# Performance work log

Hardware: AMD Instinct MI355X
Metric: run time of the kernel (lower is better)

Reference implementation:

```python
import jax, jax.numpy as jnp
import numpy as np

POOLED_H = 7
POOLED_W = 7
SPATIAL_SCALE = 0.0625
B, C, H, W = 8, 256, 48, 48
R = 300
IMG = 768  # = H / SPATIAL_SCALE


def setup_inputs() -> dict:
    key = jax.random.key(0)
    k1, k2, k3, k4 = jax.random.split(key, 4)
    features = jax.random.normal(k1, (B, C, H, W), dtype=jnp.float32)
    # rois: (batch_idx, x1, y1, x2, y2) in input-image coords
    bidx = jax.random.randint(k2, (R, 1), 0, B).astype(jnp.float32)
    tl = jax.random.uniform(k3, (R, 2), minval=0.0, maxval=IMG - 64.0)
    wh = jax.random.uniform(k4, (R, 2), minval=32.0, maxval=320.0)
    br = jnp.minimum(tl + wh, IMG - 1.0)
    rois = jnp.concatenate([bidx, tl, br], axis=1).astype(jnp.float32)
    return {"features": features, "rois": rois}


def _hat_integral(x, grid):
    """Integral from -inf to x of the unit hat basis function centered at each
    grid point g (support [g-1, g+1], peak 1, total mass 1).
    x: [..., 1-broadcastable], grid: [G] -> returns [..., G]."""
    t = x[..., None] - (grid - 1.0)
    return jnp.where(
        t <= 0.0, 0.0,
        jnp.where(t <= 1.0, 0.5 * t * t,
                  jnp.where(t <= 2.0, 1.0 - 0.5 * (2.0 - t) ** 2, 1.0)))


def reference(features, rois):
    # Precise RoI Pooling: exact double integral of the bilinear interpolant
    # over each bin, divided by bin area. Bilinear interp (with zero padding
    # outside the map, as in the CUDA PrRoIPoolingGetData) is
    #   f(u,v) = sum_{j,i} feat[j,i] * hat_j(v) * hat_i(u)
    # so the bin integral factorizes into per-axis hat-integral weights.
    Bf, Cf, Hf, Wf = features.shape
    bidx = rois[:, 0].astype(jnp.int32)
    x1 = rois[:, 1] * SPATIAL_SCALE
    y1 = rois[:, 2] * SPATIAL_SCALE
    x2 = rois[:, 3] * SPATIAL_SCALE
    y2 = rois[:, 4] * SPATIAL_SCALE
    roi_w = jnp.maximum(x2 - x1, 0.0)
    roi_h = jnp.maximum(y2 - y1, 0.0)
    bin_w = roi_w / POOLED_W  # [R]
    bin_h = roi_h / POOLED_H

    ph = jnp.arange(POOLED_H, dtype=jnp.float32)
    pw = jnp.arange(POOLED_W, dtype=jnp.float32)
    ya = y1[:, None] + ph[None, :] * bin_h[:, None]  # [R, PH]
    yb = ya + bin_h[:, None]
    xa = x1[:, None] + pw[None, :] * bin_w[:, None]  # [R, PW]
    xb = xa + bin_w[:, None]

    gy = jnp.arange(Hf, dtype=jnp.float32)
    gx = jnp.arange(Wf, dtype=jnp.float32)
    Wy = _hat_integral(yb, gy) - _hat_integral(ya, gy)  # [R, PH, H]
    Wx = _hat_integral(xb, gx) - _hat_integral(xa, gx)  # [R, PW, W]

    feat = features[bidx]  # [R, C, H, W]
    t = jnp.einsum('rpj,rcji->rcpi', Wy, feat)   # integrate over y
    num = jnp.einsum('rqi,rcpi->rcpq', Wx, t)    # integrate over x -> [R,C,PH,PW]

    area = (bin_w * bin_h)[:, None, None, None]  # win_size per ROI
    out = jnp.where(area > 0.0, num / jnp.where(area > 0.0, area, 1.0), 0.0)
    return out
```

## Files before the change

kernel.cpp:

```cpp
#include <hip/hip_runtime.h>


#define PH 7
#define PW 7
#define NBINS 49
#define SCALE 0.0625f
#define CH 256
#define FH 48
#define FW 48
#define RNUM 300
#define CB 8
#define QN 2
#define MAXJ 23
#define ROWF 28
#define PRM 112

__device__ __forceinline__ float hat_int(float x, float g) {
    float t = x - (g - 1.0f);
    if (t <= 0.0f) return 0.0f;
    if (t <= 1.0f) return 0.5f * t * t;
    if (t <= 2.0f) { float u = 2.0f - t; return 1.0f - 0.5f * u * u; }
    return 1.0f;
}

__global__ __launch_bounds__(256)
void prroi_prep(const float* __restrict__ rois, float* __restrict__ prm) {
    const int r = blockIdx.x * 4 + (threadIdx.x >> 6);
    const int t = threadIdx.x & 63;
    if (r >= RNUM || t >= 15) return;

    const float* roi = rois + r * 5;
    const int   b  = (int)roi[0];
    const float x1 = roi[1] * SCALE, y1 = roi[2] * SCALE;
    const float x2 = roi[3] * SCALE, y2 = roi[4] * SCALE;
    const float roi_w = fmaxf(x2 - x1, 0.0f), roi_h = fmaxf(y2 - y1, 0.0f);
    const float bin_w = roi_w / (float)PW, bin_h = roi_h / (float)PH;
    const float area = bin_w * bin_h;
    const float inv_area = (area > 0.0f) ? (1.0f / area) : 0.0f;

    const float ylo = fminf(y1, y2), yhi = fmaxf(y1, y2);
    const float xlo = fminf(x1, x2), xhi = fmaxf(x1, x2);
    const int j1 = min(FH - 1, (int)floorf(yhi) + 1);
    const int i1 = min(FW - 1, (int)floorf(xhi) + 1);
    const int J0 = min(max(0, (int)floorf(ylo) - 1), FH - 6);
    const int I0 = min(max(0, (int)floorf(xlo) - 1) & ~3, FW - 8);
    const int JROWS = min(FH - J0, max(j1 - J0 + 1, 6));
    int NI4 = min(((i1 - I0) >> 2) + 1, (FW - I0) >> 2);
    NI4 = max(NI4, 2);

    float* p = prm + (size_t)r * PRM;
    if (t < PH) {
        const int ph = t;
        const float ya = y1 + ph * bin_h, yb = ya + bin_h;
        const int base = min(max((int)floorf(ya) - 1, J0), J0 + JROWS - 6);
        p[84 + ph] = __int_as_float(base - J0);
#pragma unroll
        for (int k = 0; k < 6; ++k) {
            const float g = (float)(base + k);
            p[ph * 6 + k] = hat_int(yb, g) - hat_int(ya, g);
        }
    } else if (t < PH + PW) {
        const int pw = t - PH;
        const float xa = x1 + pw * bin_w, xb = xa + bin_w;
        const int base = min(max((int)floorf(xa) - 1, I0), I0 + 4 * NI4 - 6);
        p[91 + pw] = __int_as_float(base - I0);
#pragma unroll
        for (int k = 0; k < 6; ++k) {
            const float g = (float)(base + k);
            p[42 + pw * 6 + k] = hat_int(xb, g) - hat_int(xa, g);
        }
    } else {
        p[98]  = inv_area;
        p[99]  = __int_as_float(b);
        p[100] = __int_as_float(J0);
        p[101] = __int_as_float(I0);
        p[102] = __int_as_float(JROWS);
        p[103] = __int_as_float(NI4);
    }
}

__global__ __launch_bounds__(256)
void prroi_main(const float* __restrict__ feat,
                const float* __restrict__ prm,
                float* __restrict__ out) {
    const int cblk = blockIdx.x;
    const int r    = blockIdx.y;
    const int c0   = cblk * CB;
    const int tid  = threadIdx.x;

    __shared__ float patch[MAXJ * ROWF * CB];
    __shared__ float rs[PW * MAXJ * CB];

    const float* p = prm + (size_t)r * PRM;
    const int b     = __float_as_int(p[99]);
    const int J0    = __float_as_int(p[100]);
    const int I0    = __float_as_int(p[101]);
    const int JROWS = __float_as_int(p[102]);
    const int NI4   = __float_as_int(p[103]);

    const int nA = JROWS * 14;
    const int v1 = tid, v2 = tid + 256;
    int pw1 = 0, q1 = 0, j1r = 0, pw2 = 0, q2 = 0, j2r = 0, bi1 = 0, bi2 = 0;
    float wxa[6], wxb[6];
    const bool a1 = v1 < nA, a2 = v2 < nA;
    if (a1) {
        j1r = v1 / 14; const int rem = v1 - j1r * 14; pw1 = rem >> 1; q1 = rem & 1;
        bi1 = __float_as_int(p[91 + pw1]);
#pragma unroll
        for (int k = 0; k < 6; ++k) wxa[k] = p[42 + pw1 * 6 + k];
    }
    if (a2) {
        j2r = v2 / 14; const int rem = v2 - j2r * 14; pw2 = rem >> 1; q2 = rem & 1;
        bi2 = __float_as_int(p[91 + pw2]);
#pragma unroll
        for (int k = 0; k < 6; ++k) wxb[k] = p[42 + pw2 * 6 + k];
    }

    const int bin = tid & 63;
    const int cp  = tid >> 6;
    float wy[6]; int bj = 0, phv = 0, pwv = 0;
    float inv_area = p[98];
    if (bin < NBINS) {
        phv = bin / PW; pwv = bin - phv * PW;
        bj = __float_as_int(p[84 + phv]);
#pragma unroll
        for (int k = 0; k < 6; ++k) wy[k] = p[phv * 6 + k];
    }

    const float* fb = feat + (size_t)(b * CH + c0) * FH * FW;
    for (int u = tid; u < QN * MAXJ * 7; u += 256) {
        const int q   = u / (MAXJ * 7);
        const int rem = u - q * (MAXJ * 7);
        const int j   = rem / 7;
        const int i4  = rem - j * 7;
        if (j < JROWS && i4 < NI4) {
            const int ig = I0 + 4 * i4;
            const float* src = fb + ((size_t)(4 * q) * FH + (J0 + j)) * FW + ig;
            const float4 v0 = *(const float4*)(src);
            const float4 v1v = *(const float4*)(src + FH * FW);
            const float4 v2v = *(const float4*)(src + 2 * FH * FW);
            const float4 v3v = *(const float4*)(src + 3 * FH * FW);
            float* dst = &patch[((size_t)j * ROWF + 4 * i4) * CB + 4 * q];
            *(float4*)(dst + 0 * CB) = make_float4(v0.x, v1v.x, v2v.x, v3v.x);
            *(float4*)(dst + 1 * CB) = make_float4(v0.y, v1v.y, v2v.y, v3v.y);
            *(float4*)(dst + 2 * CB) = make_float4(v0.z, v1v.z, v2v.z, v3v.z);
            *(float4*)(dst + 3 * CB) = make_float4(v0.w, v1v.w, v2v.w, v3v.w);
        }
    }
    __syncthreads();

    if (a1) {
        const float* base = &patch[((size_t)j1r * ROWF + bi1) * CB + 4 * q1];
        float ax = 0.0f, ay = 0.0f, az = 0.0f, aw = 0.0f;
#pragma unroll
        for (int ii = 0; ii < 6; ++ii) {
            const float w = wxa[ii];
            const float4 v = *(const float4*)(base + ii * CB);
            ax += w * v.x; ay += w * v.y; az += w * v.z; aw += w * v.w;
        }
        *(float4*)(&rs[((size_t)pw1 * MAXJ + j1r) * CB + 4 * q1]) =
            make_float4(ax, ay, az, aw);
    }
    if (a2) {
        const float* base = &patch[((size_t)j2r * ROWF + bi2) * CB + 4 * q2];
        float ax = 0.0f, ay = 0.0f, az = 0.0f, aw = 0.0f;
#pragma unroll
        for (int ii = 0; ii < 6; ++ii) {
            const float w = wxb[ii];
            const float4 v = *(const float4*)(base + ii * CB);
            ax += w * v.x; ay += w * v.y; az += w * v.z; aw += w * v.w;
        }
        *(float4*)(&rs[((size_t)pw2 * MAXJ + j2r) * CB + 4 * q2]) =
            make_float4(ax, ay, az, aw);
    }
    __syncthreads();

    if (bin < NBINS) {
        const float* rbase = &rs[((size_t)pwv * MAXJ + bj) * CB + 2 * cp];
        float ax = 0.0f, ay = 0.0f;
#pragma unroll
        for (int jj = 0; jj < 6; ++jj) {
            const float w = wy[jj];
            const float2 v = *(const float2*)(rbase + jj * CB);
            ax += w * v.x; ay += w * v.y;
        }
        float* o = out + ((size_t)r * CH + c0 + 2 * cp) * NBINS + bin;
        o[0]     = ax * inv_area;
        o[NBINS] = ay * inv_area;
    }
}

extern "C" void kernel_launch(void* const* d_in, const int* in_sizes, int n_in,
                              void* d_out, int out_size, void* d_ws, size_t ws_size,
                              hipStream_t stream) {
    const float* feat = (const float*)d_in[0];
    const float* rois = (const float*)d_in[1];
    float* out = (float*)d_out;
    float* prm = (float*)d_ws;

    prroi_prep<<<(RNUM + 3) / 4, 256, 0, stream>>>(rois, prm);
    prroi_main<<<dim3(CH / CB, RNUM), 256, 0, stream>>>(feat, prm, out);
}
```

Measured before the change: 88.92 us.

## Fuse ROI weight prep into main kernel, computing weights in shared memory

Removes the separate prep kernel and its global workspace round-trip. Each block now recomputes the per-ROI hat-integral weights into shared memory while the feature patch loads are in flight, then reads the weights from LDS. The patch load loop is also tightened to iterate only over the rows that exist. The cost is redundant weight computation in each of the 32 channel blocks per ROI, plus fewer registers held across the phases.

```diff
diff --git a/kernel.cpp b/kernel.cpp
--- a/kernel.cpp
+++ b/kernel.cpp
@@ -10,10 +10,8 @@
 #define FW 48
 #define RNUM 300
 #define CB 8
-#define QN 2
 #define MAXJ 23
 #define ROWF 28
-#define PRM 112
 
 __device__ __forceinline__ float hat_int(float x, float g) {
     float t = x - (g - 1.0f);
@@ -24,20 +22,23 @@
 }
 
 __global__ __launch_bounds__(256)
-void prroi_prep(const float* __restrict__ rois, float* __restrict__ prm) {
-    const int r = blockIdx.x * 4 + (threadIdx.x >> 6);
-    const int t = threadIdx.x & 63;
-    if (r >= RNUM || t >= 15) return;
+void prroi_fused(const float* __restrict__ feat,
+                 const float* __restrict__ rois,
+                 float* __restrict__ out) {
+    const int cblk = blockIdx.x;
+    const int r    = blockIdx.y;
+    const int c0   = cblk * CB;
+    const int tid  = threadIdx.x;
+
+    __shared__ float patch[MAXJ * ROWF * CB];
+    __shared__ float rs[PW * MAXJ * CB];
+    __shared__ float pbuf[99];
 
     const float* roi = rois + r * 5;
-    const int   b  = (int)roi[0];
-    const float x1 = roi[1] * SCALE, y1 = roi[2] * SCALE;
-    const float x2 = roi[3] * SCALE, y2 = roi[4] * SCALE;
-    const float roi_w = fmaxf(x2 - x1, 0.0f), roi_h = fmaxf(y2 - y1, 0.0f);
-    const float bin_w = roi_w / (float)PW, bin_h = roi_h / (float)PH;
-    const float area = bin_w * bin_h;
-    const float inv_area = (area > 0.0f) ? (1.0f / area) : 0.0f;
-
+    const float f0 = roi[0], f1 = roi[1], f2 = roi[2], f3 = roi[3], f4 = roi[4];
+    const int   b  = (int)f0;
+    const float x1 = f1 * SCALE, y1 = f2 * SCALE;
+    const float x2 = f3 * SCALE, y2 = f4 * SCALE;
     const float ylo = fminf(y1, y2), yhi = fmaxf(y1, y2);
     const float xlo = fminf(x1, x2), xhi = fmaxf(x1, x2);
     const int j1 = min(FH - 1, (int)floorf(yhi) + 1);
@@ -48,95 +49,17 @@
     int NI4 = min(((i1 - I0) >> 2) + 1, (FW - I0) >> 2);
     NI4 = max(NI4, 2);
 
-    float* p = prm + (size_t)r * PRM;
-    if (t < PH) {
-        const int ph = t;
-        const float ya = y1 + ph * bin_h, yb = ya + bin_h;
-        const int base = min(max((int)floorf(ya) - 1, J0), J0 + JROWS - 6);
-        p[84 + ph] = __int_as_float(base - J0);
-#pragma unroll
-        for (int k = 0; k < 6; ++k) {
-            const float g = (float)(base + k);
-            p[ph * 6 + k] = hat_int(yb, g) - hat_int(ya, g);
-        }
-    } else if (t < PH + PW) {
-        const int pw = t - PH;
-        const float xa = x1 + pw * bin_w, xb = xa + bin_w;
-        const int base = min(max((int)floorf(xa) - 1, I0), I0 + 4 * NI4 - 6);
-        p[91 + pw] = __int_as_float(base - I0);
-#pragma unroll
-        for (int k = 0; k < 6; ++k) {
-            const float g = (float)(base + k);
-            p[42 + pw * 6 + k] = hat_int(xb, g) - hat_int(xa, g);
-        }
-    } else {
-        p[98]  = inv_area;
-        p[99]  = __int_as_float(b);
-        p[100] = __int_as_float(J0);
-        p[101] = __int_as_float(I0);
-        p[102] = __int_as_float(JROWS);
-        p[103] = __int_as_float(NI4);
-    }
-}
-
-__global__ __launch_bounds__(256)
-void prroi_main(const float* __restrict__ feat,
-                const float* __restrict__ prm,
-                float* __restrict__ out) {
-    const int cblk = blockIdx.x;
-    const int r    = blockIdx.y;
-    const int c0   = cblk * CB;
-    const int tid  = threadIdx.x;
-
-    __shared__ float patch[MAXJ * ROWF * CB];
-    __shared__ float rs[PW * MAXJ * CB];
-
-    const float* p = prm + (size_t)r * PRM;
-    const int b     = __float_as_int(p[99]);
-    const int J0    = __float_as_int(p[100]);
-    const int I0    = __float_as_int(p[101]);
-    const int JROWS = __float_as_int(p[102]);
-    const int NI4   = __float_as_int(p[103]);
-
-    const int nA = JROWS * 14;
-    const int v1 = tid, v2 = tid + 256;
-    int pw1 = 0, q1 = 0, j1r = 0, pw2 = 0, q2 = 0, j2r = 0, bi1 = 0, bi2 = 0;
-    float wxa[6], wxb[6];
-    const bool a1 = v1 < nA, a2 = v2 < nA;
-    if (a1) {
-        j1r = v1 / 14; const int rem = v1 - j1r * 14; pw1 = rem >> 1; q1 = rem & 1;
-        bi1 = __float_as_int(p[91 + pw1]);
-#pragma unroll
-        for (int k = 0; k < 6; ++k) wxa[k] = p[42 + pw1 * 6 + k];
-    }
-    if (a2) {
-        j2r = v2 / 14; const int rem = v2 - j2r * 14; pw2 = rem >> 1; q2 = rem & 1;
-        bi2 = __float_as_int(p[91 + pw2]);
-#pragma unroll
-        for (int k = 0; k < 6; ++k) wxb[k] = p[42 + pw2 * 6 + k];
-    }
-
-    const int bin = tid & 63;
-    const int cp  = tid >> 6;
-    float wy[6]; int bj = 0, phv = 0, pwv = 0;
-    float inv_area = p[98];
-    if (bin < NBINS) {
-        phv = bin / PW; pwv = bin - phv * PW;
-        bj = __float_as_int(p[84 + phv]);
-#pragma unroll
-        for (int k = 0; k < 6; ++k) wy[k] = p[phv * 6 + k];
-    }
-
     const float* fb = feat + (size_t)(b * CH + c0) * FH * FW;
-    for (int u = tid; u < QN * MAXJ * 7; u += 256) {
-        const int q   = u / (MAXJ * 7);
-        const int rem = u - q * (MAXJ * 7);
-        const int j   = rem / 7;
-        const int i4  = rem - j * 7;
-        if (j < JROWS && i4 < NI4) {
+    const int J7 = JROWS * 7;
+    for (int u = tid; u < 2 * J7; u += 256) {
+        const int q  = (u >= J7) ? 1 : 0;
+        const int rm = u - q * J7;
+        const int j  = rm / 7;
+        const int i4 = rm - j * 7;
+        if (i4 < NI4) {
             const int ig = I0 + 4 * i4;
             const float* src = fb + ((size_t)(4 * q) * FH + (J0 + j)) * FW + ig;
-            const float4 v0 = *(const float4*)(src);
+            const float4 v0  = *(const float4*)(src);
             const float4 v1v = *(const float4*)(src + FH * FW);
             const float4 v2v = *(const float4*)(src + 2 * FH * FW);
             const float4 v3v = *(const float4*)(src + 3 * FH * FW);
@@ -147,40 +70,87 @@
             *(float4*)(dst + 3 * CB) = make_float4(v0.w, v1v.w, v2v.w, v3v.w);
         }
     }
-    __syncthreads();
 
-    if (a1) {
-        const float* base = &patch[((size_t)j1r * ROWF + bi1) * CB + 4 * q1];
-        float ax = 0.0f, ay = 0.0f, az = 0.0f, aw = 0.0f;
+    if (tid < PH) {
+        const float roi_h = fmaxf(y2 - y1, 0.0f);
+        const float bin_h = roi_h / (float)PH;
+        const int ph = tid;
+        const float ya = y1 + ph * bin_h, yb = ya + bin_h;
+        const int base = min(max((int)floorf(ya) - 1, J0), J0 + JROWS - 6);
+        pbuf[84 + ph] = __int_as_float(base - J0);
 #pragma unroll
-        for (int ii = 0; ii < 6; ++ii) {
-            const float w = wxa[ii];
-            const float4 v = *(const float4*)(base + ii * CB);
-            ax += w * v.x; ay += w * v.y; az += w * v.z; aw += w * v.w;
+        for (int k = 0; k < 6; ++k) {
+            const float g = (float)(base + k);
+            pbuf[ph * 6 + k] = hat_int(yb, g) - hat_int(ya, g);
         }
-        *(float4*)(&rs[((size_t)pw1 * MAXJ + j1r) * CB + 4 * q1]) =
-            make_float4(ax, ay, az, aw);
-    }
-    if (a2) {
-        const float* base = &patch[((size_t)j2r * ROWF + bi2) * CB + 4 * q2];
-        float ax = 0.0f, ay = 0.0f, az = 0.0f, aw = 0.0f;
+    } else if (tid < PH + PW) {
+        const float roi_w = fmaxf(x2 - x1, 0.0f);
+        const float bin_w = roi_w / (float)PW;
+        const int pw = tid - PH;
+        const float xa = x1 + pw * bin_w, xb = xa + bin_w;
+        const int base = min(max((int)floorf(xa) - 1, I0), I0 + 4 * NI4 - 6);
+        pbuf[91 + pw] = __int_as_float(base - I0);
 #pragma unroll
-        for (int ii = 0; ii < 6; ++ii) {
-            const float w = wxb[ii];
-            const float4 v = *(const float4*)(base + ii * CB);
-            ax += w * v.x; ay += w * v.y; az += w * v.z; aw += w * v.w;
+        for (int k = 0; k < 6; ++k) {
+            const float g = (float)(base + k);
+            pbuf[42 + pw * 6 + k] = hat_int(xb, g) - hat_int(xa, g);
         }
-        *(float4*)(&rs[((size_t)pw2 * MAXJ + j2r) * CB + 4 * q2]) =
-            make_float4(ax, ay, az, aw);
+    } else if (tid == PH + PW) {
+        const float roi_w = fmaxf(x2 - x1, 0.0f);
+        const float roi_h = fmaxf(y2 - y1, 0.0f);
+        const float area = (roi_w / (float)PW) * (roi_h / (float)PH);
+        pbuf[98] = (area > 0.0f) ? (1.0f / area) : 0.0f;
     }
     __syncthreads();
 
+    const int nA = JROWS * 14;
+    {
+        const int v1 = tid;
+        if (v1 < nA) {
+            const int j = v1 / 14; const int rem = v1 - j * 14;
+            const int pw = rem >> 1, q = rem & 1;
+            const int bi = __float_as_int(pbuf[91 + pw]);
+            const float* base = &patch[((size_t)j * ROWF + bi) * CB + 4 * q];
+            float ax = 0.0f, ay = 0.0f, az = 0.0f, aw = 0.0f;
+#pragma unroll
+            for (int ii = 0; ii < 6; ++ii) {
+                const float w = pbuf[42 + pw * 6 + ii];
+                const float4 v = *(const float4*)(base + ii * CB);
+                ax += w * v.x; ay += w * v.y; az += w * v.z; aw += w * v.w;
+            }
+            *(float4*)(&rs[((size_t)pw * MAXJ + j) * CB + 4 * q]) =
+                make_float4(ax, ay, az, aw);
+        }
+        const int v2 = tid + 256;
+        if (v2 < nA) {
+            const int j = v2 / 14; const int rem = v2 - j * 14;
+            const int pw = rem >> 1, q = rem & 1;
+            const int bi = __float_as_int(pbuf[91 + pw]);
+            const float* base = &patch[((size_t)j * ROWF + bi) * CB + 4 * q];
+            float ax = 0.0f, ay = 0.0f, az = 0.0f, aw = 0.0f;
+#pragma unroll
+            for (int ii = 0; ii < 6; ++ii) {
+                const float w = pbuf[42 + pw * 6 + ii];
+                const float4 v = *(const float4*)(base + ii * CB);
+                ax += w * v.x; ay += w * v.y; az += w * v.z; aw += w * v.w;
+            }
+            *(float4*)(&rs[((size_t)pw * MAXJ + j) * CB + 4 * q]) =
+                make_float4(ax, ay, az, aw);
+        }
+    }
+    __syncthreads();
+
+    const int bin = tid & 63;
+    const int cp  = tid >> 6;
     if (bin < NBINS) {
+        const int phv = bin / PW, pwv = bin - phv * PW;
+        const int bj = __float_as_int(pbuf[84 + phv]);
+        const float inv_area = pbuf[98];
         const float* rbase = &rs[((size_t)pwv * MAXJ + bj) * CB + 2 * cp];
         float ax = 0.0f, ay = 0.0f;
 #pragma unroll
         for (int jj = 0; jj < 6; ++jj) {
-            const float w = wy[jj];
+            const float w = pbuf[phv * 6 + jj];
             const float2 v = *(const float2*)(rbase + jj * CB);
             ax += w * v.x; ay += w * v.y;
         }
@@ -196,8 +166,7 @@
     const float* feat = (const float*)d_in[0];
     const float* rois = (const float*)d_in[1];
     float* out = (float*)d_out;
-    float* prm = (float*)d_ws;
+    (void)d_ws; (void)ws_size;
 
-    prroi_prep<<<(RNUM + 3) / 4, 256, 0, stream>>>(rois, prm);
-    prroi_main<<<dim3(CH / CB, RNUM), 256, 0, stream>>>(feat, prm, out);
+    prroi_fused<<<dim3(CH / CB, RNUM), 256, 0, stream>>>(feat, rois, out);
 }
```

Result: slower. 92.31 us (+3.8%).

## Give each wavefront its own channel pair and drop block barriers

Applied to the files above, without the earlier changes.

Restructures the main kernel so each of the four wavefronts in a block handles two channels independently, with a private LDS patch and row-sum buffer. Block-wide __syncthreads are replaced by s_waitcnt lgkmcnt(0), since only one wavefront touches each buffer. The patch uses a float2 layout with an XOR swizzle to reduce LDS bank conflicts, and launch bounds request 6 waves per SIMD. Each wave now issues narrower loads (two channels per float4 pair) and does more serial row iterations per lane, which may lower memory-level parallelism per block.

```diff
diff --git a/kernel.cpp b/kernel.cpp
--- a/kernel.cpp
+++ b/kernel.cpp
@@ -9,11 +9,10 @@
 #define FH 48
 #define FW 48
 #define RNUM 300
-#define CB 8
-#define QN 2
 #define MAXJ 23
-#define ROWF 28
 #define PRM 112
+#define PATCHF (MAXJ * 28 * 2)
+#define RSF 328
 
 __device__ __forceinline__ float hat_int(float x, float g) {
     float t = x - (g - 1.0f);
@@ -79,17 +78,19 @@
     }
 }
 
-__global__ __launch_bounds__(256)
+__global__ __launch_bounds__(256, 6)
 void prroi_main(const float* __restrict__ feat,
                 const float* __restrict__ prm,
                 float* __restrict__ out) {
-    const int cblk = blockIdx.x;
+    const int wv   = threadIdx.x >> 6;
+    const int lane = threadIdx.x & 63;
     const int r    = blockIdx.y;
-    const int c0   = cblk * CB;
-    const int tid  = threadIdx.x;
+    const int cblk = blockIdx.x * 4 + wv;
+    const int c0   = cblk * 2;
 
-    __shared__ float patch[MAXJ * ROWF * CB];
-    __shared__ float rs[PW * MAXJ * CB];
+    __shared__ float lds[4][PATCHF + RSF];
+    float* patch = lds[wv];
+    float* rsw   = lds[wv] + PATCHF;
 
     const float* p = prm + (size_t)r * PRM;
     const int b     = __float_as_int(p[99]);
@@ -97,96 +98,71 @@
     const int I0    = __float_as_int(p[101]);
     const int JROWS = __float_as_int(p[102]);
     const int NI4   = __float_as_int(p[103]);
+    const float ia  = p[98];
 
-    const int nA = JROWS * 14;
-    const int v1 = tid, v2 = tid + 256;
-    int pw1 = 0, q1 = 0, j1r = 0, pw2 = 0, q2 = 0, j2r = 0, bi1 = 0, bi2 = 0;
-    float wxa[6], wxb[6];
-    const bool a1 = v1 < nA, a2 = v2 < nA;
-    if (a1) {
-        j1r = v1 / 14; const int rem = v1 - j1r * 14; pw1 = rem >> 1; q1 = rem & 1;
-        bi1 = __float_as_int(p[91 + pw1]);
+    const int pwA = lane >> 3;
+    const int jsl = lane & 7;
+    const bool actA = lane < 56;
+    float wx[6]; int bi = 0;
+    if (actA) {
+        bi = __float_as_int(p[91 + pwA]);
 #pragma unroll
-        for (int k = 0; k < 6; ++k) wxa[k] = p[42 + pw1 * 6 + k];
+        for (int k = 0; k < 6; ++k) wx[k] = p[42 + pwA * 6 + k];
     }
-    if (a2) {
-        j2r = v2 / 14; const int rem = v2 - j2r * 14; pw2 = rem >> 1; q2 = rem & 1;
-        bi2 = __float_as_int(p[91 + pw2]);
+    const bool actB = lane < NBINS;
+    int bj = 0, pwB = 0;
+    float wy[6];
+    if (actB) {
+        const int ph = lane / 7;
+        pwB = lane - ph * 7;
+        bj = __float_as_int(p[84 + ph]);
 #pragma unroll
-        for (int k = 0; k < 6; ++k) wxb[k] = p[42 + pw2 * 6 + k];
+        for (int k = 0; k < 6; ++k) wy[k] = p[ph * 6 + k];
     }
 
-    const int bin = tid & 63;
-    const int cp  = tid >> 6;
-    float wy[6]; int bj = 0, phv = 0, pwv = 0;
-    float inv_area = p[98];
-    if (bin < NBINS) {
-        phv = bin / PW; pwv = bin - phv * PW;
-        bj = __float_as_int(p[84 + phv]);
-#pragma unroll
-        for (int k = 0; k < 6; ++k) wy[k] = p[phv * 6 + k];
-    }
-
-    const float* fb = feat + (size_t)(b * CH + c0) * FH * FW;
-    for (int u = tid; u < QN * MAXJ * 7; u += 256) {
-        const int q   = u / (MAXJ * 7);
-        const int rem = u - q * (MAXJ * 7);
-        const int j   = rem / 7;
-        const int i4  = rem - j * 7;
-        if (j < JROWS && i4 < NI4) {
-            const int ig = I0 + 4 * i4;
-            const float* src = fb + ((size_t)(4 * q) * FH + (J0 + j)) * FW + ig;
-            const float4 v0 = *(const float4*)(src);
-            const float4 v1v = *(const float4*)(src + FH * FW);
-            const float4 v2v = *(const float4*)(src + 2 * FH * FW);
-            const float4 v3v = *(const float4*)(src + 3 * FH * FW);
-            float* dst = &patch[((size_t)j * ROWF + 4 * i4) * CB + 4 * q];
-            *(float4*)(dst + 0 * CB) = make_float4(v0.x, v1v.x, v2v.x, v3v.x);
-            *(float4*)(dst + 1 * CB) = make_float4(v0.y, v1v.y, v2v.y, v3v.y);
-            *(float4*)(dst + 2 * CB) = make_float4(v0.z, v1v.z, v2v.z, v3v.z);
-            *(float4*)(dst + 3 * CB) = make_float4(v0.w, v1v.w, v2v.w, v3v.w);
+    const float* fb = feat + (size_t)(b * CH + c0) * (FH * FW);
+    const int NU = JROWS << 3;
+    for (int u = lane; u < NU; u += 64) {
+        const int j = u >> 3, i4 = u & 7;
+        if (i4 < NI4) {
+            const float* src = fb + (size_t)(J0 + j) * FW + I0 + 4 * i4;
+            const float4 a = *(const float4*)src;
+            const float4 c = *(const float4*)(src + FH * FW);
+            const int base = j * 56 + 8 * i4;
+            const int sw = (j & 7) << 1;
+            *(float2*)&patch[(base + 0) ^ sw] = make_float2(a.x, c.x);
+            *(float2*)&patch[(base + 2) ^ sw] = make_float2(a.y, c.y);
+            *(float2*)&patch[(base + 4) ^ sw] = make_float2(a.z, c.z);
+            *(float2*)&patch[(base + 6) ^ sw] = make_float2(a.w, c.w);
         }
     }
-    __syncthreads();
+    asm volatile("s_waitcnt lgkmcnt(0)" ::: "memory");
 
-    if (a1) {
-        const float* base = &patch[((size_t)j1r * ROWF + bi1) * CB + 4 * q1];
-        float ax = 0.0f, ay = 0.0f, az = 0.0f, aw = 0.0f;
+    if (actA) {
+        for (int j = jsl; j < JROWS; j += 8) {
+            const int rowb = j * 56 + 2 * bi;
+            const int sw = (j & 7) << 1;
+            float ax = 0.0f, ay = 0.0f;
 #pragma unroll
-        for (int ii = 0; ii < 6; ++ii) {
-            const float w = wxa[ii];
-            const float4 v = *(const float4*)(base + ii * CB);
-            ax += w * v.x; ay += w * v.y; az += w * v.z; aw += w * v.w;
+            for (int ii = 0; ii < 6; ++ii) {
+                const float2 v = *(const float2*)&patch[(rowb + 2 * ii) ^ sw];
+                ax += wx[ii] * v.x; ay += wx[ii] * v.y;
+            }
+            *(float2*)&rsw[(pwA * MAXJ + j) * 2] = make_float2(ax, ay);
         }
-        *(float4*)(&rs[((size_t)pw1 * MAXJ + j1r) * CB + 4 * q1]) =
-            make_float4(ax, ay, az, aw);
     }
-    if (a2) {
-        const float* base = &patch[((size_t)j2r * ROWF + bi2) * CB + 4 * q2];
-        float ax = 0.0f, ay = 0.0f, az = 0.0f, aw = 0.0f;
-#pragma unroll
-        for (int ii = 0; ii < 6; ++ii) {
-            const float w = wxb[ii];
-            const float4 v = *(const float4*)(base + ii * CB);
-            ax += w * v.x; ay += w * v.y; az += w * v.z; aw += w * v.w;
-        }
-        *(float4*)(&rs[((size_t)pw2 * MAXJ + j2r) * CB + 4 * q2]) =
-            make_float4(ax, ay, az, aw);
-    }
-    __syncthreads();
+    asm volatile("s_waitcnt lgkmcnt(0)" ::: "memory");
 
-    if (bin < NBINS) {
-        const float* rbase = &rs[((size_t)pwv * MAXJ + bj) * CB + 2 * cp];
+    if (actB) {
         float ax = 0.0f, ay = 0.0f;
 #pragma unroll
         for (int jj = 0; jj < 6; ++jj) {
-            const float w = wy[jj];
-            const float2 v = *(const float2*)(rbase + jj * CB);
-            ax += w * v.x; ay += w * v.y;
+            const float2 v = *(const float2*)&rsw[(pwB * MAXJ + (bj + jj)) * 2];
+            ax += wy[jj] * v.x; ay += wy[jj] * v.y;
         }
-        float* o = out + ((size_t)r * CH + c0 + 2 * cp) * NBINS + bin;
-        o[0]     = ax * inv_area;
-        o[NBINS] = ay * inv_area;
+        float* o = out + ((size_t)r * CH + c0) * NBINS + lane;
+        o[0]     = ax * ia;
+        o[NBINS] = ay * ia;
     }
 }
 
@@ -199,5 +175,5 @@
     float* prm = (float*)d_ws;
 
     prroi_prep<<<(RNUM + 3) / 4, 256, 0, stream>>>(rois, prm);
-    prroi_main<<<dim3(CH / CB, RNUM), 256, 0, stream>>>(feat, prm, out);
+    prroi_main<<<dim3(32, RNUM), 256, 0, stream>>>(feat, prm, out);
 }
```

Result: faster. 86.36 us (-2.9%).
